# Kernel optimization log

Measured on AMD Instinct MI355X. Metric: run time of the kernel, lower is better.

The kernel has to match this reference:

```python
import jax, jax.numpy as jnp
import numpy as np

DIM = 512
NSLOTS = 8
ITERS = 3
EPS = 1e-8
LN_EPS = 1e-5
SCALE = DIM ** -0.5


def _ln(x, g, b):
    m = jnp.mean(x, axis=-1, keepdims=True)
    v = jnp.mean((x - m) ** 2, axis=-1, keepdims=True)
    return (x - m) / jnp.sqrt(v + LN_EPS) * g + b


def _gru(x, h, W_ih, W_hh, b_ih, b_hh):
    # PyTorch GRUCell, gate order r,z,n
    gi = x @ W_ih.T + b_ih
    gh = h @ W_hh.T + b_hh
    ir, iz, inn = jnp.split(gi, 3, axis=-1)
    hr, hz, hn = jnp.split(gh, 3, axis=-1)
    r = jax.nn.sigmoid(ir + hr)
    z = jax.nn.sigmoid(iz + hz)
    n = jnp.tanh(inn + r * hn)
    return (1.0 - z) * n + z * h


def _norm_attn(dots):
    # softmax over slot axis, then renormalize over token axis
    a = jax.nn.softmax(dots, axis=1)
    return a / (jnp.sum(a, axis=-1, keepdims=True) + EPS)


def setup_inputs() -> dict:
    key = jax.random.key(0)
    ks = jax.random.split(key, 16)
    b, na, ni = 32, 1024, 3136
    d, hd = DIM, DIM  # hidden_dim = max(dim, 128) = 512
    s = 0.02
    inp = {
        'inputs_audio': jax.random.normal(ks[0], (b, na, d), jnp.float32),
        'inputs_image': jax.random.normal(ks[1], (b, ni, d), jnp.float32),
        'slots_noise': jax.random.normal(ks[2], (b, NSLOTS, d), jnp.float32),
        'slots_mu': jax.random.normal(ks[3], (1, 1, d), jnp.float32),
        'slots_logsigma': jnp.zeros((1, 1, d), jnp.float32),
        'ln_in_g': jnp.ones((d,), jnp.float32), 'ln_in_b': jnp.zeros((d,), jnp.float32),
        'ln_slots_g': jnp.ones((d,), jnp.float32), 'ln_slots_b': jnp.zeros((d,), jnp.float32),
        'ln_ff_g': jnp.ones((d,), jnp.float32), 'ln_ff_b': jnp.zeros((d,), jnp.float32),
        'Wq': jax.random.normal(ks[4], (d, d), jnp.float32) * s, 'bq': jnp.zeros((d,), jnp.float32),
        'Wk': jax.random.normal(ks[5], (d, d), jnp.float32) * s, 'bk': jnp.zeros((d,), jnp.float32),
        'Wv': jax.random.normal(ks[6], (d, d), jnp.float32) * s, 'bv': jnp.zeros((d,), jnp.float32),
        'W_ih': jax.random.normal(ks[7], (3 * d, d), jnp.float32) * s,
        'W_hh': jax.random.normal(ks[8], (3 * d, d), jnp.float32) * s,
        'b_ih': jnp.zeros((3 * d,), jnp.float32), 'b_hh': jnp.zeros((3 * d,), jnp.float32),
        'W1': jax.random.normal(ks[9], (hd, d), jnp.float32) * s, 'b1': jnp.zeros((hd,), jnp.float32),
        'W2': jax.random.normal(ks[10], (d, hd), jnp.float32) * s, 'b2': jnp.zeros((d,), jnp.float32),
    }
    return inp


def reference(inputs_audio, inputs_image, slots_noise, slots_mu, slots_logsigma,
              ln_in_g, ln_in_b, ln_slots_g, ln_slots_b, ln_ff_g, ln_ff_b,
              Wq, bq, Wk, bk, Wv, bv, W_ih, W_hh, b_ih, b_hh, W1, b1, W2, b2):
    b, na, d = inputs_audio.shape
    slots0 = slots_mu + jnp.exp(slots_logsigma) * slots_noise  # [b, S, d]

    ia = _ln(inputs_audio, ln_in_g, ln_in_b)
    ii = _ln(inputs_image, ln_in_g, ln_in_b)
    k_a = ia @ Wk.T + bk
    v_a = ia @ Wv.T + bv
    k_i = ii @ Wk.T + bk
    v_i = ii @ Wv.T + bv

    def mlp(x):
        return jax.nn.relu(x @ W1.T + b1) @ W2.T + b2

    def step(slots, k, v):
        prev = slots
        sn = _ln(slots, ln_slots_g, ln_slots_b)
        q = sn @ Wq.T + bq
        dots = jnp.einsum('bid,bjd->bij', q, k) * SCALE
        attn = _norm_attn(dots)
        upd = jnp.einsum('bjd,bij->bid', v, attn)
        h = _gru(upd.reshape(-1, d), prev.reshape(-1, d), W_ih, W_hh, b_ih, b_hh)
        slots = h.reshape(b, -1, d)
        slots = slots + mlp(_ln(slots, ln_ff_g, ln_ff_b))
        return slots, q, attn

    slots_a, slots_i = slots0, slots0
    for _ in range(ITERS):
        slots_a, q_a, attn_a = step(slots_a, k_a, v_a)
        slots_i, q_i, attn_i = step(slots_i, k_i, v_i)

    cross_ai = _norm_attn(jnp.einsum('bid,bjd->bij', q_a, k_i) * SCALE)  # audio->image
    cross_ia = _norm_attn(jnp.einsum('bid,bjd->bij', q_i, k_a) * SCALE)  # image->audio

    return (slots_a, q_a, k_a, attn_a, cross_ia,
            slots_i, q_i, k_i, attn_i, cross_ai)
```

## Files before the change

kernel.cpp:

```cpp
#include <hip/hip_runtime.h>
#include <hip/hip_bf16.h>

#define DIM 512
#define EPS 1e-8f
#define LN_EPS 1e-5f
#define SCALE 0.04419417382415922f

typedef float f32x4 __attribute__((ext_vector_type(4)));
typedef __bf16 bf16;
typedef __bf16 bf16x8 __attribute__((ext_vector_type(8)));

typedef const __attribute__((address_space(1))) void gvoid;
typedef __attribute__((address_space(3))) void lvoid;

__device__ inline float bf2f_lo(unsigned u) { union { unsigned x; float f; } c; c.x = u << 16; return c.f; }
__device__ inline float bf2f_hi(unsigned u) { union { unsigned x; float f; } c; c.x = u & 0xffff0000u; return c.f; }

#define SBAR() do { __builtin_amdgcn_sched_barrier(0); \
                    __builtin_amdgcn_s_barrier(); \
                    __builtin_amdgcn_sched_barrier(0); } while (0)

__global__ __launch_bounds__(256) void k_stats_convert(
    const float* __restrict__ xa, const float* __restrict__ xi,
    bf16* __restrict__ xbfa, bf16* __restrict__ xbfi,
    float* __restrict__ sa, float* __restrict__ si, int MA)
{
  int row = blockIdx.x * 4 + (threadIdx.x >> 6);
  int lane = threadIdx.x & 63;
  bool isA = row < MA;
  int lrow = isA ? row : row - MA;
  const float* xr = (isA ? xa : xi) + (size_t)lrow * DIM;
  bf16* xbf = (isA ? xbfa : xbfi) + (size_t)lrow * DIM;
  float* stats = (isA ? sa : si) + (size_t)lrow * 2;
  float4 a = *(const float4*)(xr + lane * 8);
  float4 b = *(const float4*)(xr + lane * 8 + 4);
  float s  = a.x + a.y + a.z + a.w + b.x + b.y + b.z + b.w;
  float ss = a.x*a.x + a.y*a.y + a.z*a.z + a.w*a.w
           + b.x*b.x + b.y*b.y + b.z*b.z + b.w*b.w;
  for (int off = 32; off; off >>= 1) { s += __shfl_xor(s, off); ss += __shfl_xor(ss, off); }
  float mean = s * (1.0f / DIM);
  float var  = ss * (1.0f / DIM) - mean * mean;
  float rs   = rsqrtf(var + LN_EPS);
  if (lane == 0) { stats[0] = mean; stats[1] = rs; }
  union { bf16 h[8]; uint4 u; } cv;
  cv.h[0] = (bf16)a.x; cv.h[1] = (bf16)a.y; cv.h[2] = (bf16)a.z; cv.h[3] = (bf16)a.w;
  cv.h[4] = (bf16)b.x; cv.h[5] = (bf16)b.y; cv.h[6] = (bf16)b.z; cv.h[7] = (bf16)b.w;
  *(uint4*)(xbf + lane * 8) = cv.u;
}

__global__ __launch_bounds__(256) void k_stats512(
    const float* __restrict__ x, float* __restrict__ stats)
{
  int row = blockIdx.x * 4 + (threadIdx.x >> 6);
  int lane = threadIdx.x & 63;
  const float* xr = x + (size_t)row * DIM;
  float4 a = *(const float4*)(xr + lane * 8);
  float4 b = *(const float4*)(xr + lane * 8 + 4);
  float s  = a.x + a.y + a.z + a.w + b.x + b.y + b.z + b.w;
  float ss = a.x*a.x + a.y*a.y + a.z*a.z + a.w*a.w
           + b.x*b.x + b.y*b.y + b.z*b.z + b.w*b.w;
  for (int off = 32; off; off >>= 1) { s += __shfl_xor(s, off); ss += __shfl_xor(ss, off); }
  float mean = s * (1.0f / DIM);
  float rs   = rsqrtf(ss * (1.0f / DIM) - mean * mean + LN_EPS);
  if (lane == 0) { stats[row * 2] = mean; stats[row * 2 + 1] = rs; }
}

__global__ __launch_bounds__(64) void k_prep(
    const float* __restrict__ Wk, const float* __restrict__ bk,
    const float* __restrict__ Wv, const float* __restrict__ bv,
    const float* __restrict__ g_in, const float* __restrict__ b_in,
    const float* __restrict__ Wq, const float* __restrict__ bq,
    const float* __restrict__ g_s, const float* __restrict__ b_s,
    const float* __restrict__ W1, const float* __restrict__ b1,
    const float* __restrict__ g_f, const float* __restrict__ b_f,
    bf16* __restrict__ wbf, float* __restrict__ c1kv, float* __restrict__ c2kv,
    float* __restrict__ Wqp, float* __restrict__ cq1, float* __restrict__ cq2,
    float* __restrict__ W1p, float* __restrict__ cf1, float* __restrict__ cf2)
{
  int n = blockIdx.x; int lane = threadIdx.x;
  if (n < 1024) {
    const float* W = (n < DIM) ? (Wk + (size_t)n * DIM) : (Wv + (size_t)(n - DIM) * DIM);
    float bias = (n < DIM) ? bk[n] : bv[n - DIM];
    float s1 = 0.f, s2 = 0.f;
    union { bf16 h[8]; uint4 u; } cv;
#pragma unroll
    for (int j = 0; j < 8; ++j) {
      int d = lane * 8 + j;
      float w = W[d];
      float gw = g_in[d] * w;
      s1 += gw; s2 += b_in[d] * w;
      cv.h[j] = (bf16)gw;
    }
    *(uint4*)(wbf + (size_t)n * DIM + lane * 8) = cv.u;
    for (int off = 32; off; off >>= 1) { s1 += __shfl_xor(s1, off); s2 += __shfl_xor(s2, off); }
    if (lane == 0) { c1kv[n] = s1; c2kv[n] = s2 + bias; }
  } else {
    int m; const float* W; float bias; const float* g; const float* b;
    float* Wp; float* cc1; float* cc2;
    if (n < 1536) { m = n - 1024; W = Wq + (size_t)m * DIM; bias = bq[m]; g = g_s; b = b_s; Wp = Wqp; cc1 = cq1; cc2 = cq2; }
    else          { m = n - 1536; W = W1 + (size_t)m * DIM; bias = b1[m]; g = g_f; b = b_f; Wp = W1p; cc1 = cf1; cc2 = cf2; }
    float s1 = 0.f, s2 = 0.f;
    float arr[8];
#pragma unroll
    for (int j = 0; j < 8; ++j) {
      int d = lane * 8 + j;
      float w = W[d];
      float gw = g[d] * w;
      s1 += gw; s2 += b[d] * w;
      arr[j] = gw;
    }
    *(float4*)(Wp + (size_t)m * DIM + lane * 8)     = make_float4(arr[0], arr[1], arr[2], arr[3]);
    *(float4*)(Wp + (size_t)m * DIM + lane * 8 + 4) = make_float4(arr[4], arr[5], arr[6], arr[7]);
    for (int off = 32; off; off >>= 1) { s1 += __shfl_xor(s1, off); s2 += __shfl_xor(s2, off); }
    if (lane == 0) { cc1[m] = s1; cc2[m] = s2 + bias; }
  }
}

// ... 97 lines not shown
      pk.h[0] = (bf16)o.x; pk.h[1] = (bf16)o.y; pk.h[2] = (bf16)o.z; pk.h[3] = (bf16)o.w;
      if (col0 < DIM) {
        *(float4*)&kout[(size_t)row * DIM + col] = o;
        if (kbf) *(uint2*)&kbf[(size_t)row * DIM + col] = pk.u;
      } else {
        *(uint2*)&vbf[(size_t)row * DIM + (col - DIM)] = pk.u;
      }
    }
  }
}

__global__ __launch_bounds__(256) void k_f2bf(
    const float* __restrict__ in, bf16* __restrict__ out)
{
  size_t i = ((size_t)blockIdx.x * 256 + threadIdx.x) * 8;
  float4 a = *(const float4*)(in + i);
  float4 b = *(const float4*)(in + i + 4);
  union { bf16 h[8]; uint4 u; } cv;
  cv.h[0] = (bf16)a.x; cv.h[1] = (bf16)a.y; cv.h[2] = (bf16)a.z; cv.h[3] = (bf16)a.w;
  cv.h[4] = (bf16)b.x; cv.h[5] = (bf16)b.y; cv.h[6] = (bf16)b.z; cv.h[7] = (bf16)b.w;
  *(uint4*)(out + i) = cv.u;
}

__global__ __launch_bounds__(256) void k_init_slots(
    const float* __restrict__ noise, const float* __restrict__ mu,
    const float* __restrict__ lsig, float* __restrict__ slots,
    float* __restrict__ stats)
{
  int row = blockIdx.x;
  int t = threadIdx.x;
  int d1 = t + 256;
  float v0 = mu[t]  + expf(lsig[t])  * noise[row * DIM + t];
  float v1 = mu[d1] + expf(lsig[d1]) * noise[row * DIM + d1];
  slots[(size_t)row * DIM + t]  = v0;
  slots[(size_t)row * DIM + d1] = v1;
  slots[131072 + (size_t)row * DIM + t]  = v0;
  slots[131072 + (size_t)row * DIM + d1] = v1;
  float s = v0 + v1, ss = v0 * v0 + v1 * v1;
  for (int off = 32; off; off >>= 1) { s += __shfl_xor(s, off); ss += __shfl_xor(ss, off); }
  __shared__ float red[8];
  int wv = t >> 6, ln = t & 63;
  if (ln == 0) { red[wv] = s; red[4 + wv] = ss; }
  __syncthreads();
  if (t == 0) {
    s = red[0] + red[1] + red[2] + red[3];
    ss = red[4] + red[5] + red[6] + red[7];
    float mean = s * (1.0f / DIM);
    float rs = rsqrtf(ss * (1.0f / DIM) - mean * mean + LN_EPS);
    stats[row * 2] = mean; stats[row * 2 + 1] = rs;
    stats[(row + 256) * 2] = mean; stats[(row + 256) * 2 + 1] = rs;
  }
}

template <int MODE>
__global__ __launch_bounds__(128) void k_sgemm(
    const float* __restrict__ A, const float* __restrict__ B, int N,
    float* __restrict__ C,
    const float* __restrict__ c1a, const float* __restrict__ c2a,
    const float* __restrict__ stats,
    const float* __restrict__ bias, const float* __restrict__ invden,
    const float* __restrict__ R,
    float* __restrict__ outA, float* __restrict__ outI,
    bf16* __restrict__ qbf)
{
  __shared__ float As[32][33];
  __shared__ float Bs[64][33];
  int t = threadIdx.x;
  int m0 = blockIdx.y * 32, n0 = blockIdx.x * 64;
  float acc[4][4] = {};
  for (int k0 = 0; k0 < DIM; k0 += 32) {
    __syncthreads();
#pragma unroll
    for (int p = 0; p < 2; ++p) {
      int idx = p * 128 + t, r = idx >> 3, c4 = (idx & 7) * 4;
      float4 v = *(const float4*)(A + (size_t)(m0 + r) * DIM + k0 + c4);
      As[r][c4] = v.x; As[r][c4 + 1] = v.y; As[r][c4 + 2] = v.z; As[r][c4 + 3] = v.w;
    }
#pragma unroll
    for (int p = 0; p < 4; ++p) {
      int idx = p * 128 + t, r = idx >> 3, c4 = (idx & 7) * 4;
      float4 v = *(const float4*)(B + (size_t)(n0 + r) * DIM + k0 + c4);
      Bs[r][c4] = v.x; Bs[r][c4 + 1] = v.y; Bs[r][c4 + 2] = v.z; Bs[r][c4 + 3] = v.w;
    }
    __syncthreads();
    int tr = t >> 4, tc = t & 15;
#pragma unroll
    for (int k = 0; k < 32; ++k) {
      float a0 = As[tr * 4][k], a1 = As[tr * 4 + 1][k], a2 = As[tr * 4 + 2][k], a3 = As[tr * 4 + 3][k];
      float b0 = Bs[tc * 4][k], b1 = Bs[tc * 4 + 1][k], b2 = Bs[tc * 4 + 2][k], b3 = Bs[tc * 4 + 3][k];
      acc[0][0] += a0 * b0; acc[0][1] += a0 * b1; acc[0][2] += a0 * b2; acc[0][3] += a0 * b3;
      acc[1][0] += a1 * b0; acc[1][1] += a1 * b1; acc[1][2] += a1 * b2; acc[1][3] += a1 * b3;
      acc[2][0] += a2 * b0; acc[2][1] += a2 * b1; acc[2][2] += a2 * b2; acc[2][3] += a2 * b3;
      acc[3][0] += a3 * b0; acc[3][1] += a3 * b1; acc[3][2] += a3 * b2; acc[3][3] += a3 * b3;
    }
  }
  int tr = t >> 4, tc = t & 15;
#pragma unroll
  for (int mi = 0; mi < 4; ++mi) {
    int row = m0 + tr * 4 + mi;
#pragma unroll
    for (int ni = 0; ni < 4; ++ni) {
      int col = n0 + tc * 4 + ni;
      float v = acc[mi][ni];
      if (MODE == 0 || MODE == 3) {
        float mean = stats[row * 2], rs = stats[row * 2 + 1];
        v = rs * v - rs * mean * c1a[col] + c2a[col];
      }
      if (MODE == 4) v += bias[col];
      if (MODE == 3) v = fmaxf(v, 0.0f);
      if (MODE == 4) v += R[(size_t)row * N + col];
      if (MODE == 0) {
        if (outA) {
          if (row < 256) outA[(size_t)row * DIM + col] = v;
          else           outI[(size_t)(row - 256) * DIM + col] = v;
        }
        qbf[(size_t)row * DIM + col] = (bf16)(v * SCALE);
      } else {
        C[(size_t)row * N + col] = v;
        if (MODE == 4 && outA) {
          if (row < 256) outA[(size_t)row * DIM + col] = v;
          else           outI[(size_t)(row - 256) * DIM + col] = v;
        }
      }
    }
  }
}

__global__ __launch_bounds__(128) void k_gates(
    const float* __restrict__ num, const float* __restrict__ slots,
    const float* __restrict__ Wih, const float* __restrict__ Whh,
    const float* __restrict__ bih, const float* __restrict__ bhh,
    const float* __restrict__ invden,
    float* __restrict__ gib, float* __restrict__ ghb)
{
  bool first = blockIdx.x < 24;
  const float* A = first ? num : slots;
  const float* B = first ? Wih : Whh;
  const float* bias = first ? bih : bhh;
  float* C = first ? gib : ghb;
  int n0 = (first ? blockIdx.x : blockIdx.x - 24) * 64;
  int m0 = blockIdx.y * 32;
  __shared__ float As[32][33];
  __shared__ float Bs[64][33];
  int t = threadIdx.x;
  float acc[4][4] = {};
  for (int k0 = 0; k0 < DIM; k0 += 32) {
    __syncthreads();
#pragma unroll
    for (int p = 0; p < 2; ++p) {
      int idx = p * 128 + t, r = idx >> 3, c4 = (idx & 7) * 4;
      float4 v = *(const float4*)(A + (size_t)(m0 + r) * DIM + k0 + c4);
      As[r][c4] = v.x; As[r][c4 + 1] = v.y; As[r][c4 + 2] = v.z; As[r][c4 + 3] = v.w;
    }
#pragma unroll
    for (int p = 0; p < 4; ++p) {
      int idx = p * 128 + t, r = idx >> 3, c4 = (idx & 7) * 4;
      float4 v = *(const float4*)(B + (size_t)(n0 + r) * DIM + k0 + c4);
      Bs[r][c4] = v.x; Bs[r][c4 + 1] = v.y; Bs[r][c4 + 2] = v.z; Bs[r][c4 + 3] = v.w;
    }
    __syncthreads();
    int tr = t >> 4, tc = t & 15;
#pragma unroll
    for (int k = 0; k < 32; ++k) {
      float a0 = As[tr * 4][k], a1 = As[tr * 4 + 1][k], a2 = As[tr * 4 + 2][k], a3 = As[tr * 4 + 3][k];
      float b0 = Bs[tc * 4][k], b1 = Bs[tc * 4 + 1][k], b2 = Bs[tc * 4 + 2][k], b3 = Bs[tc * 4 + 3][k];
      acc[0][0] += a0 * b0; acc[0][1] += a0 * b1; acc[0][2] += a0 * b2; acc[0][3] += a0 * b3;
      acc[1][0] += a1 * b0; acc[1][1] += a1 * b1; acc[1][2] += a1 * b2; acc[1][3] += a1 * b3;
      acc[2][0] += a2 * b0; acc[2][1] += a2 * b1; acc[2][2] += a2 * b2; acc[2][3] += a2 * b3;
      acc[3][0] += a3 * b0; acc[3][1] += a3 * b1; acc[3][2] += a3 * b2; acc[3][3] += a3 * b3;
    }
  }
  int tr = t >> 4, tc = t & 15;
#pragma unroll
  for (int mi = 0; mi < 4; ++mi) {
    int row = m0 + tr * 4 + mi;
    float sc = first ? invden[row] : 1.0f;
#pragma unroll
    for (int ni = 0; ni < 4; ++ni) {
      int col = n0 + tc * 4 + ni;
      C[(size_t)row * 1536 + col] = acc[mi][ni] * sc + bias[col];
    }
  }
}

template <int LAST>
__global__ __launch_bounds__(256) void k_dots_upd(
    const bf16* __restrict__ qA, const bf16* __restrict__ qI,
    const bf16* __restrict__ kA, const bf16* __restrict__ kI,
    const bf16* __restrict__ vA, const bf16* __restrict__ vI,
    float* __restrict__ aoutA, float* __restrict__ aoutI,
    float* __restrict__ acA, float* __restrict__ acI,
    float* __restrict__ denp, float* __restrict__ denpc,
    float* __restrict__ numpA, float* __restrict__ numpI,
    int NA_, int NI_)
{
  __shared__ bf16 ks[2][128 * 64];
  __shared__ float ash[128 * 12];
  __shared__ float dsh[64];
  int t = threadIdx.x, wave = t >> 6, lane = t & 63;
  int b = blockIdx.y, tile = blockIdx.x;
  bool isA = tile < 8;
  int til = isA ? tile : tile - 8;
  int N = isA ? NA_ : NI_;
  int nc = isA ? 8 : 25;
  int j0 = til * 128;
  const bf16* qo = (isA ? qA : qI) + (size_t)b * 8 * DIM;
  const bf16* qc = (isA ? qI : qA) + (size_t)b * 8 * DIM;
  const bf16* k  = (isA ? kA : kI) + (size_t)b * N * DIM;
  const bf16* v  = (isA ? vA : vI) + (size_t)b * N * DIM;
  float* aout = (isA ? aoutA : aoutI) + (LAST ? (size_t)b * 8 * N : 0);
  float* aco  = (isA ? acA  : acI ) + (LAST ? (size_t)b * 8 * N : 0);
  int drow = (isA ? 0 : 256) + b * 8;

  const int l15 = lane & 15, q16 = lane >> 4;
  bf16x8 afq[16], afqc[16];
  {
    const bf16* qr = qo + (size_t)(l15 & 7) * DIM + q16 * 8;
#pragma unroll
    for (int f = 0; f < 16; ++f) afq[f] = *(const bf16x8*)(qr + f * 32);
  }
  if (LAST) {
    const bf16* qr = qc + (size_t)(l15 & 7) * DIM + q16 * 8;
#pragma unroll
    for (int f = 0; f < 16; ++f) afqc[f] = *(const bf16x8*)(qr + f * 32);
  }

  const int sr  = wave * 8 + (lane >> 3);
  const int sgl = ((lane & 7) ^ (lane >> 3)) * 8;
  int jr = j0 + sr; if (jr > N - 1) jr = N - 1;
  const bf16* ksrc = k + (size_t)jr * DIM + sgl;
  int jr2 = j0 + 32 + sr; if (jr2 > N - 1) jr2 = N - 1;
  const bf16* ksrc2 = k + (size_t)jr2 * DIM + sgl;
  int jr3 = j0 + 64 + sr; if (jr3 > N - 1) jr3 = N - 1;
// ... 83 lines not shown
    if (LAST) {
      float dv[8];
#pragma unroll
      for (int r = 0; r < 4; ++r) {
        float own = accc[n][r];
        float oth = __shfl_xor(own, 16);
        if (q16 == 0) { dv[r] = own; dv[4 + r] = oth; }
        else          { dv[r] = oth; dv[4 + r] = own; }
      }
      float mx = dv[0];
#pragma unroll
      for (int i = 1; i < 8; ++i) mx = fmaxf(mx, dv[i]);
      float sum = 0.f;
#pragma unroll
      for (int i = 0; i < 8; ++i) { dv[i] = __expf(dv[i] - mx); sum += dv[i]; }
      float inv = 1.0f / sum;
#pragma unroll
      for (int i = 0; i < 8; ++i) {
        float av = valid ? dv[i] * inv : 0.0f;
        dsumc[i] += av;
        if (q16 == 0 && valid) aco[(size_t)i * N + j] = av;
      }
    }
  }
#pragma unroll
  for (int i = 0; i < 8; ++i) {
    float x1 = dsum[i];
    x1 += __shfl_xor(x1, 1); x1 += __shfl_xor(x1, 2);
    x1 += __shfl_xor(x1, 4); x1 += __shfl_xor(x1, 8);
    dsum[i] = x1;
    if (LAST) {
      float x2 = dsumc[i];
      x2 += __shfl_xor(x2, 1); x2 += __shfl_xor(x2, 2);
      x2 += __shfl_xor(x2, 4); x2 += __shfl_xor(x2, 8);
      dsumc[i] = x2;
    }
  }
  if (lane == 0) {
#pragma unroll
    for (int i = 0; i < 8; ++i) {
      dsh[wave * 8 + i] = dsum[i];
      if (LAST) dsh[32 + wave * 8 + i] = dsumc[i];
    }
  }
  __syncthreads();
  if (t < 8) {
    denp[((size_t)drow + t) * 32 + til] = dsh[t] + dsh[8 + t] + dsh[16 + t] + dsh[24 + t];
  }
  if (LAST && t >= 8 && t < 16) {
    int i = t - 8;
    denpc[((size_t)drow + i) * 32 + til] = dsh[32 + i] + dsh[40 + i] + dsh[48 + i] + dsh[56 + i];
  }

  float ua[16] = {};
  int d0 = t * 2;
  for (int jj = 0; jj < 128; ++jj) {
    int jv = j0 + jj; if (jv > N - 1) jv = N - 1;
    unsigned vv = *(const unsigned*)(v + (size_t)jv * DIM + d0);
    float v0 = bf2f_lo(vv), v1 = bf2f_hi(vv);
    float4 a0 = *(const float4*)&ash[jj * 12];
    float4 a1 = *(const float4*)&ash[jj * 12 + 4];
    ua[0]  += a0.x * v0; ua[1]  += a0.x * v1;
    ua[2]  += a0.y * v0; ua[3]  += a0.y * v1;
    ua[4]  += a0.z * v0; ua[5]  += a0.z * v1;
    ua[6]  += a0.w * v0; ua[7]  += a0.w * v1;
    ua[8]  += a1.x * v0; ua[9]  += a1.x * v1;
    ua[10] += a1.y * v0; ua[11] += a1.y * v1;
    ua[12] += a1.z * v0; ua[13] += a1.z * v1;
    ua[14] += a1.w * v0; ua[15] += a1.w * v1;
  }
  float* np = (isA ? numpA : numpI) + (((size_t)b * nc + til) * 8) * DIM;
#pragma unroll
  for (int i = 0; i < 8; ++i)
    *(float2*)&np[(size_t)i * DIM + d0] = make_float2(ua[i * 2], ua[i * 2 + 1]);
}

__global__ __launch_bounds__(256) void k_numred(
    const float* __restrict__ numpA, const float* __restrict__ numpI,
    const float* __restrict__ denp,
    float* __restrict__ num, float* __restrict__ invden)
{
  int m = blockIdx.x, t = threadIdx.x;
  bool isA = m < 256;
  int mm = isA ? m : m - 256;
  int bb = mm >> 3, i = mm & 7;
  int nc = isA ? 8 : 25;
  const float* np = (isA ? numpA : numpI) + (((size_t)bb * nc) * 8 + i) * DIM;
  int d0 = t * 2;
  float s0 = 0.f, s1 = 0.f;
  for (int c = 0; c < nc; ++c) {
    float2 vv = *(const float2*)&np[(size_t)c * 8 * DIM + d0];
    s0 += vv.x; s1 += vv.y;
  }
  *(float2*)&num[(size_t)m * DIM + d0] = make_float2(s0, s1);
  if (t == 0) {
    float den = EPS;
    for (int c2 = 0; c2 < nc; ++c2) den += denp[(size_t)m * 32 + c2];
    invden[m] = 1.0f / den;
  }
}

__global__ __launch_bounds__(256) void k_gru(
    const float* __restrict__ gi, const float* __restrict__ gh,
    const float* __restrict__ prev,
    float* __restrict__ hout, float* __restrict__ stats_h)
{
  int m = blockIdx.x; int t = threadIdx.x;
  size_t b3 = (size_t)m * 1536, b1 = (size_t)m * DIM;
  float h[2]; float s = 0.f, ss = 0.f;
#pragma unroll
  for (int p = 0; p < 2; ++p) {
    int d = t + p * 256;
    float ir = gi[b3 + d], iz = gi[b3 + 512 + d], in_ = gi[b3 + 1024 + d];
    float hr = gh[b3 + d], hz = gh[b3 + 512 + d], hn = gh[b3 + 1024 + d];
    float r = 1.f / (1.f + __expf(-(ir + hr)));
    float z = 1.f / (1.f + __expf(-(iz + hz)));
    float n = tanhf(in_ + r * hn);
    float hv = (1.f - z) * n + z * prev[b1 + d];
    hout[b1 + d] = hv;
    h[p] = hv; s += hv; ss += hv * hv;
  }
  for (int off = 32; off; off >>= 1) { s += __shfl_xor(s, off); ss += __shfl_xor(ss, off); }
  __shared__ float red[8];
  int wv = t >> 6, ln = t & 63;
  if (ln == 0) { red[wv] = s; red[4 + wv] = ss; }
  __syncthreads();
  s = red[0] + red[1] + red[2] + red[3];
  ss = red[4] + red[5] + red[6] + red[7];
  float mean = s * (1.0f / DIM);
  float rs = rsqrtf(ss * (1.0f / DIM) - mean * mean + LN_EPS);
  if (t == 0) { stats_h[m * 2] = mean; stats_h[m * 2 + 1] = rs; }
}

__global__ __launch_bounds__(256) void k_renorm2(
    const float* __restrict__ aA, const float* __restrict__ aI,
    const float* __restrict__ denp,
    float* __restrict__ outA, float* __restrict__ outI, int NA_, int NI_)
{
  int m = blockIdx.x; int t = threadIdx.x;
  bool isA = m < 256;
  int mm = isA ? m : m - 256;
  int N = isA ? NA_ : NI_;
  int nch = isA ? 8 : 25;
  const float* in = (isA ? aA : aI) + (size_t)mm * N;
  float* out = (isA ? outA : outI) + (size_t)mm * N;
  float den = EPS;
  for (int c = 0; c < nch; ++c) den += denp[(size_t)m * 32 + c];
  float inv = 1.0f / den;
  for (int idx = t; idx * 4 < N; idx += 256) {
    float4 v = *(const float4*)&in[idx * 4];
    v.x *= inv; v.y *= inv; v.z *= inv; v.w *= inv;
    *(float4*)&out[idx * 4] = v;
  }
}

extern "C" void kernel_launch(void* const* d_in, const int* in_sizes, int n_in,
                              void* d_out, int out_size, void* d_ws, size_t ws_size,
                              hipStream_t stream)
{
  (void)in_sizes; (void)n_in; (void)out_size;
  const float* x_a   = (const float*)d_in[0];
  const float* x_i   = (const float*)d_in[1];
  const float* noise = (const float*)d_in[2];
  const float* mu    = (const float*)d_in[3];
  const float* lsig  = (const float*)d_in[4];
  const float* ln_in_g = (const float*)d_in[5];
  const float* ln_in_b = (const float*)d_in[6];
  const float* ln_s_g  = (const float*)d_in[7];
  const float* ln_s_b  = (const float*)d_in[8];
  const float* ln_f_g  = (const float*)d_in[9];
  const float* ln_f_b  = (const float*)d_in[10];
  const float* Wq = (const float*)d_in[11]; const float* bq = (const float*)d_in[12];
  const float* Wk = (const float*)d_in[13]; const float* bk = (const float*)d_in[14];
  const float* Wv = (const float*)d_in[15]; const float* bv = (const float*)d_in[16];
  const float* W_ih = (const float*)d_in[17]; const float* W_hh = (const float*)d_in[18];
  const float* b_ih = (const float*)d_in[19]; const float* b_hh = (const float*)d_in[20];
  const float* W1 = (const float*)d_in[21]; const float* b1 = (const float*)d_in[22];
  const float* W2 = (const float*)d_in[23]; const float* b2 = (const float*)d_in[24];

  const int NA = 1024, NI = 3136;
  const int MA = 32 * NA, MI = 32 * NI;

  float* out = (float*)d_out;
  float* o_slots_a  = out;
  float* o_q_a      = out + 131072;
  float* o_k_a      = out + 262144;
  float* o_attn_a   = out + 17039360;
  float* o_cross_ia = out + 17301504;
  float* o_slots_i  = out + 17563648;
  float* o_q_i      = out + 17694720;
  float* o_k_i      = out + 17825792;
  float* o_attn_i   = out + 69206016;
  float* o_cross_ai = out + 70008832;

  char* w = (char*)d_ws;
  size_t used = 0;
  auto alloc = [&](size_t bytes) {
    char* p = w + used;
    used += (bytes + 255) & ~(size_t)255;
    return p;
  };
  bf16* xbf_a = (bf16*)alloc((size_t)MA * DIM * 2);
  bf16* xbf_i = (bf16*)alloc((size_t)MI * DIM * 2);
  bf16* vbf_a = (bf16*)alloc((size_t)MA * DIM * 2);
  bf16* vbf_i = (bf16*)alloc((size_t)MI * DIM * 2);
  float* stats_a = (float*)alloc((size_t)MA * 2 * 4);
  float* stats_i = (float*)alloc((size_t)MI * 2 * 4);
  bf16* wbf  = (bf16*)alloc(1024 * 512 * 2);
  float* c1kv = (float*)alloc(1024 * 4);
  float* c2kv = (float*)alloc(1024 * 4);
  float* Wqp = (float*)alloc(512 * 512 * 4);
  float* cq1 = (float*)alloc(512 * 4);
  float* cq2 = (float*)alloc(512 * 4);
  float* W1p = (float*)alloc(512 * 512 * 4);
  float* cf1 = (float*)alloc(512 * 4);
  float* cf2 = (float*)alloc(512 * 4);
  float* slots = (float*)alloc(512 * 512 * 4);
  bf16*  qbf   = (bf16*)alloc(512 * 512 * 2);
  float* mid   = (float*)alloc(512 * 512 * 4);
  float* hid   = (float*)alloc(512 * 512 * 4);
  float* num   = (float*)alloc(512 * 512 * 4);
  float* gib   = (float*)alloc(512 * 1536 * 4);
  float* ghb   = (float*)alloc(512 * 1536 * 4);
  float* stats_s = (float*)alloc(512 * 2 * 4);
  float* stats_h = (float*)alloc(512 * 2 * 4);
  float* invden  = (float*)alloc(512 * 4);
  float* denp    = (float*)alloc(512 * 32 * 4);
  float* denpc   = (float*)alloc(512 * 32 * 4);
  float* abuf_a  = (float*)alloc((size_t)256 * NA * 4);
  float* abuf_i  = (float*)alloc((size_t)256 * NI * 4);
  float* abufc_a = (float*)alloc((size_t)256 * NA * 4);
  float* abufc_i = (float*)alloc((size_t)256 * NI * 4);
  float* numpA   = (float*)alloc((size_t)32 * 8 * 8 * DIM * 4);
  float* numpI   = (float*)alloc((size_t)32 * 25 * 8 * DIM * 4);
  if (used > ws_size) return;

  size_t kbf_bytes = (((size_t)MA * DIM * 2 + 255) & ~(size_t)255)
                   + (((size_t)MI * DIM * 2 + 255) & ~(size_t)255);
  bf16* kbf_a; bf16* kbf_i; bool kbf_fused;
  if (used + kbf_bytes <= ws_size) {
    kbf_a = (bf16*)alloc((size_t)MA * DIM * 2);
    kbf_i = (bf16*)alloc((size_t)MI * DIM * 2);
    kbf_fused = true;
  } else {
    kbf_a = xbf_a; kbf_i = xbf_i;
    kbf_fused = false;
  }

  k_stats_convert<<<(MA + MI) / 4, 256, 0, stream>>>(x_a, x_i, xbf_a, xbf_i,
                                                     stats_a, stats_i, MA);
  k_prep<<<2048, 64, 0, stream>>>(Wk, bk, Wv, bv, ln_in_g, ln_in_b,
                                  Wq, bq, ln_s_g, ln_s_b, W1, b1, ln_f_g, ln_f_b,
                                  wbf, c1kv, c2kv, Wqp, cq1, cq2, W1p, cf1, cf2);
  {
    int nblkA = (MA / 128) * 8;
    int nblkTot = nblkA + (MI / 128) * 8;
    k_kv_gemm<<<nblkTot, 256, 0, stream>>>(xbf_a, xbf_i, wbf, stats_a, stats_i,
        c1kv, c2kv, o_k_a, o_k_i,
        kbf_fused ? kbf_a : nullptr, kbf_fused ? kbf_i : nullptr,
        vbf_a, vbf_i, nblkA, nblkTot);
  }
  if (!kbf_fused) {
    k_f2bf<<<MA * DIM / 2048, 256, 0, stream>>>(o_k_a, kbf_a);
    k_f2bf<<<MI * DIM / 2048, 256, 0, stream>>>(o_k_i, kbf_i);
  }
  k_init_slots<<<256, 256, 0, stream>>>(noise, mu, lsig, slots, stats_s);

  for (int it = 0; it < 3; ++it) {
    bool last = (it == 2);
    k_sgemm<0><<<dim3(8, 16), 128, 0, stream>>>(slots, Wqp, DIM, nullptr,
        cq1, cq2, stats_s, nullptr, nullptr, nullptr,
        last ? o_q_a : nullptr, last ? o_q_i : nullptr, qbf);
    if (!last)
      k_dots_upd<0><<<dim3(33, 32), 256, 0, stream>>>(qbf, qbf + 256 * DIM,
          kbf_a, kbf_i, vbf_a, vbf_i,
          nullptr, nullptr, nullptr, nullptr, denp, nullptr,
          numpA, numpI, NA, NI);
    else
      k_dots_upd<1><<<dim3(33, 32), 256, 0, stream>>>(qbf, qbf + 256 * DIM,
          kbf_a, kbf_i, vbf_a, vbf_i,
          abuf_a, abuf_i, abufc_a, abufc_i, denp, denpc,
          numpA, numpI, NA, NI);
    k_numred<<<512, 256, 0, stream>>>(numpA, numpI, denp, num, invden);
    k_gates<<<dim3(48, 16), 128, 0, stream>>>(num, slots, W_ih, W_hh,
        b_ih, b_hh, invden, gib, ghb);
    k_gru<<<512, 256, 0, stream>>>(gib, ghb, slots, mid, stats_h);
    k_sgemm<3><<<dim3(8, 16), 128, 0, stream>>>(mid, W1p, DIM, hid,
        cf1, cf2, stats_h, nullptr, nullptr, nullptr, nullptr, nullptr, nullptr);
    k_sgemm<4><<<dim3(8, 16), 128, 0, stream>>>(hid, W2, DIM, slots,
        nullptr, nullptr, nullptr, b2, nullptr, mid,
        last ? o_slots_a : nullptr, last ? o_slots_i : nullptr, nullptr);
    if (!last) k_stats512<<<128, 256, 0, stream>>>(slots, stats_s);
  }

  k_renorm2<<<512, 256, 0, stream>>>(abuf_a, abuf_i, denp, o_attn_a, o_attn_i, NA, NI);
  k_renorm2<<<512, 256, 0, stream>>>(abufc_a, abufc_i, denpc, o_cross_ia, o_cross_ai, NA, NI);
}
```

Baseline: 1.104 ms.

## Fuse per-iteration slot update chain into one persistent kernel with grid barriers

Replaces the numred, gates, GRU, two MLP GEMMs, stats and next-iteration Q GEMM launches with a single 256-block persistent kernel that separates phases with atomic-counter grid barriers. The Q projection for the next iteration is folded into the end of the chain, and the first Q GEMM is hoisted before the loop. The goal is to remove several small kernel launches and their gaps per iteration. The cost is spin-wait barriers that assume all 256 blocks are co-resident, plus smaller 32x64 tiles with 2 outputs per thread, which leave many blocks idle in the 128-tile phases.

```diff
diff --git a/kernel.cpp b/kernel.cpp
--- a/kernel.cpp
+++ b/kernel.cpp
@@ -19,6 +19,17 @@
 #define SBAR() do { __builtin_amdgcn_sched_barrier(0); \
                     __builtin_amdgcn_s_barrier(); \
                     __builtin_amdgcn_sched_barrier(0); } while (0)
+
+__device__ inline void gsync(unsigned* bar) {
+  __syncthreads();
+  __threadfence();
+  if (threadIdx.x == 0) {
+    atomicAdd(bar, 1u);
+    while (atomicAdd(bar, 0u) < 256u) __builtin_amdgcn_s_sleep(2);
+  }
+  __syncthreads();
+  __threadfence();
+}
 
 __global__ __launch_bounds__(256) void k_stats_convert(
     const float* __restrict__ xa, const float* __restrict__ xi,
@@ -46,23 +57,6 @@
   cv.h[0] = (bf16)a.x; cv.h[1] = (bf16)a.y; cv.h[2] = (bf16)a.z; cv.h[3] = (bf16)a.w;
   cv.h[4] = (bf16)b.x; cv.h[5] = (bf16)b.y; cv.h[6] = (bf16)b.z; cv.h[7] = (bf16)b.w;
   *(uint4*)(xbf + lane * 8) = cv.u;
-}
-
-__global__ __launch_bounds__(256) void k_stats512(
-    const float* __restrict__ x, float* __restrict__ stats)
-{
-  int row = blockIdx.x * 4 + (threadIdx.x >> 6);
-  int lane = threadIdx.x & 63;
-  const float* xr = x + (size_t)row * DIM;
-  float4 a = *(const float4*)(xr + lane * 8);
-  float4 b = *(const float4*)(xr + lane * 8 + 4);
-  float s  = a.x + a.y + a.z + a.w + b.x + b.y + b.z + b.w;
-  float ss = a.x*a.x + a.y*a.y + a.z*a.z + a.w*a.w
-           + b.x*b.x + b.y*b.y + b.z*b.z + b.w*b.w;
-  for (int off = 32; off; off >>= 1) { s += __shfl_xor(s, off); ss += __shfl_xor(ss, off); }
-  float mean = s * (1.0f / DIM);
-  float rs   = rsqrtf(ss * (1.0f / DIM) - mean * mean + LN_EPS);
-  if (lane == 0) { stats[row * 2] = mean; stats[row * 2 + 1] = rs; }
 }
 
 __global__ __launch_bounds__(64) void k_prep(
@@ -266,16 +260,10 @@
   }
 }
 
-template <int MODE>
-__global__ __launch_bounds__(128) void k_sgemm(
-    const float* __restrict__ A, const float* __restrict__ B, int N,
-    float* __restrict__ C,
+__global__ __launch_bounds__(128) void k_qgemm(
+    const float* __restrict__ A, const float* __restrict__ B,
     const float* __restrict__ c1a, const float* __restrict__ c2a,
-    const float* __restrict__ stats,
-    const float* __restrict__ bias, const float* __restrict__ invden,
-    const float* __restrict__ R,
-    float* __restrict__ outA, float* __restrict__ outI,
-    bf16* __restrict__ qbf)
+    const float* __restrict__ stats, bf16* __restrict__ qbf)
 {
   __shared__ float As[32][33];
   __shared__ float Bs[64][33];
@@ -312,87 +300,232 @@
 #pragma unroll
   for (int mi = 0; mi < 4; ++mi) {
     int row = m0 + tr * 4 + mi;
+    float mean = stats[row * 2], rs = stats[row * 2 + 1];
 #pragma unroll
     for (int ni = 0; ni < 4; ++ni) {
       int col = n0 + tc * 4 + ni;
-      float v = acc[mi][ni];
-      if (MODE == 0 || MODE == 3) {
-        float mean = stats[row * 2], rs = stats[row * 2 + 1];
-        v = rs * v - rs * mean * c1a[col] + c2a[col];
+      float v = rs * acc[mi][ni] - rs * mean * c1a[col] + c2a[col];
+      qbf[(size_t)row * DIM + col] = (bf16)(v * SCALE);
+    }
+  }
+}
+
+__device__ inline void mm32x64(
+    const float* __restrict__ A, const float* __restrict__ B,
+    int m0, int n0, float acc[4][2],
+    float (*As)[33], float (*Bs)[33])
+{
+  int t = threadIdx.x;
+#pragma unroll
+  for (int i = 0; i < 4; ++i) { acc[i][0] = 0.f; acc[i][1] = 0.f; }
+  for (int k0 = 0; k0 < DIM; k0 += 32) {
+    __syncthreads();
+    {
+      int r = t >> 3, c4 = (t & 7) * 4;
+      float4 v = *(const float4*)(A + (size_t)(m0 + r) * DIM + k0 + c4);
+      As[r][c4] = v.x; As[r][c4 + 1] = v.y; As[r][c4 + 2] = v.z; As[r][c4 + 3] = v.w;
+    }
+#pragma unroll
+    for (int p = 0; p < 2; ++p) {
+      int idx = p * 256 + t, r = idx >> 3, c4 = (idx & 7) * 4;
+      float4 v = *(const float4*)(B + (size_t)(n0 + r) * DIM + k0 + c4);
+      Bs[r][c4] = v.x; Bs[r][c4 + 1] = v.y; Bs[r][c4 + 2] = v.z; Bs[r][c4 + 3] = v.w;
+    }
+    __syncthreads();
+    int tr = t >> 5, tc = t & 31;
+#pragma unroll
+    for (int k = 0; k < 32; ++k) {
+      float a0 = As[tr * 4][k], a1 = As[tr * 4 + 1][k];
+      float a2 = As[tr * 4 + 2][k], a3 = As[tr * 4 + 3][k];
+      float b0 = Bs[tc * 2][k], b1 = Bs[tc * 2 + 1][k];
+      acc[0][0] += a0 * b0; acc[0][1] += a0 * b1;
+      acc[1][0] += a1 * b0; acc[1][1] += a1 * b1;
+      acc[2][0] += a2 * b0; acc[2][1] += a2 * b1;
+      acc[3][0] += a3 * b0; acc[3][1] += a3 * b1;
+    }
+  }
+}
+
+template <int CMODE>
+__global__ __launch_bounds__(256) void k_chain(
+    const float* __restrict__ numpA, const float* __restrict__ numpI,
+    const float* __restrict__ denp,
+    float* __restrict__ num, float* __restrict__ invden,
+    const float* __restrict__ Wih, const float* __restrict__ Whh,
+    const float* __restrict__ bih, const float* __restrict__ bhh,
+    float* __restrict__ gib, float* __restrict__ ghb,
+    float* __restrict__ slots, float* __restrict__ mid,
+    float* __restrict__ stats_h,
+    const float* __restrict__ W1p, const float* __restrict__ cf1,
+    const float* __restrict__ cf2, float* __restrict__ hid,
+    const float* __restrict__ W2, const float* __restrict__ b2,
+    const float* __restrict__ Wqp, const float* __restrict__ cq1,
+    const float* __restrict__ cq2,
+    float* __restrict__ stats_s, bf16* __restrict__ qbf,
+    float* __restrict__ o_slots_a, float* __restrict__ o_slots_i,
+    float* __restrict__ o_q_a, float* __restrict__ o_q_i,
+    unsigned* __restrict__ bar)
+{
+  __shared__ float As[32][33];
+  __shared__ float Bs[64][33];
+  __shared__ float red[8];
+  int t = threadIdx.x;
+
+  {
+    int r0 = blockIdx.x * 2;
+    for (int r = r0; r < r0 + 2; ++r) {
+      bool isA = r < 256;
+      int mm = isA ? r : r - 256;
+      int bb = mm >> 3, i = mm & 7;
+      int nc = isA ? 8 : 25;
+      const float* np = (isA ? numpA : numpI) + (((size_t)bb * nc) * 8 + i) * DIM;
+      int d0 = t * 2;
+      float s0 = 0.f, s1 = 0.f;
+      for (int c = 0; c < nc; ++c) {
+        float2 vv = *(const float2*)&np[(size_t)c * 8 * DIM + d0];
+        s0 += vv.x; s1 += vv.y;
       }
-      if (MODE == 4) v += bias[col];
-      if (MODE == 3) v = fmaxf(v, 0.0f);
-      if (MODE == 4) v += R[(size_t)row * N + col];
-      if (MODE == 0) {
-        if (outA) {
-          if (row < 256) outA[(size_t)row * DIM + col] = v;
-          else           outI[(size_t)(row - 256) * DIM + col] = v;
-        }
+      *(float2*)&num[(size_t)r * DIM + d0] = make_float2(s0, s1);
+      if (t == 0) {
+        float den = EPS;
+        for (int c2 = 0; c2 < nc; ++c2) den += denp[(size_t)r * 32 + c2];
+        invden[r] = 1.0f / den;
+      }
+    }
+  }
+  gsync(bar + 0);
+
+  for (int vt = blockIdx.x; vt < 768; vt += 256) {
+    bool first = vt < 384;
+    int lv = first ? vt : vt - 384;
+    int m0 = (lv / 24) * 32, n0 = (lv % 24) * 64;
+    const float* Aa = first ? num : slots;
+    const float* Bb = first ? Wih : Whh;
+    const float* bias = first ? bih : bhh;
+    float* C = first ? gib : ghb;
+    float acc[4][2];
+    mm32x64(Aa, Bb, m0, n0, acc, As, Bs);
+    int tr = t >> 5, tc = t & 31;
+#pragma unroll
+    for (int i = 0; i < 4; ++i) {
+      int row = m0 + tr * 4 + i;
+      float sc = first ? invden[row] : 1.0f;
+      float2 o = make_float2(acc[i][0] * sc + bias[n0 + tc * 2],
+                             acc[i][1] * sc + bias[n0 + tc * 2 + 1]);
+      *(float2*)&C[(size_t)row * 1536 + n0 + tc * 2] = o;
+    }
+  }
+  gsync(bar + 1);
+
+  for (int rr = 0; rr < 2; ++rr) {
+    int m = blockIdx.x * 2 + rr;
+    size_t b3 = (size_t)m * 1536, b1 = (size_t)m * DIM;
+    float h[2]; float s = 0.f, ss = 0.f;
+#pragma unroll
+    for (int p = 0; p < 2; ++p) {
+      int d = t + p * 256;
+      float ir = gib[b3 + d], iz = gib[b3 + 512 + d], in_ = gib[b3 + 1024 + d];
+      float hr = ghb[b3 + d], hz = ghb[b3 + 512 + d], hn = ghb[b3 + 1024 + d];
+      float r = 1.f / (1.f + __expf(-(ir + hr)));
+      float z = 1.f / (1.f + __expf(-(iz + hz)));
+      float n = tanhf(in_ + r * hn);
+      float hv = (1.f - z) * n + z * slots[b1 + d];
+      mid[b1 + d] = hv;
+      h[p] = hv; s += hv; ss += hv * hv;
+    }
+    for (int off = 32; off; off >>= 1) { s += __shfl_xor(s, off); ss += __shfl_xor(ss, off); }
+    int wv = t >> 6, ln = t & 63;
+    if (ln == 0) { red[wv] = s; red[4 + wv] = ss; }
+    __syncthreads();
+    if (t == 0) {
+      s = red[0] + red[1] + red[2] + red[3];
+      ss = red[4] + red[5] + red[6] + red[7];
+      float mean = s * (1.0f / DIM);
+      float rs = rsqrtf(ss * (1.0f / DIM) - mean * mean + LN_EPS);
+      stats_h[m * 2] = mean; stats_h[m * 2 + 1] = rs;
+    }
+    __syncthreads();
+  }
+  gsync(bar + 2);
+
+  for (int vt = blockIdx.x; vt < 128; vt += 256) {
+    int m0 = (vt >> 3) * 32, n0 = (vt & 7) * 64;
+    float acc[4][2];
+    mm32x64(mid, W1p, m0, n0, acc, As, Bs);
+    int tr = t >> 5, tc = t & 31;
+#pragma unroll
+    for (int i = 0; i < 4; ++i) {
+      int row = m0 + tr * 4 + i;
+      float mean = stats_h[row * 2], rs = stats_h[row * 2 + 1];
+      float2 o;
+      o.x = fmaxf(rs * acc[i][0] - rs * mean * cf1[n0 + tc * 2]     + cf2[n0 + tc * 2],     0.f);
+      o.y = fmaxf(rs * acc[i][1] - rs * mean * cf1[n0 + tc * 2 + 1] + cf2[n0 + tc * 2 + 1], 0.f);
+      *(float2*)&hid[(size_t)row * DIM + n0 + tc * 2] = o;
+    }
+  }
+  gsync(bar + 3);
+
+  for (int vt = blockIdx.x; vt < 128; vt += 256) {
+    int m0 = (vt >> 3) * 32, n0 = (vt & 7) * 64;
+    float acc[4][2];
+    mm32x64(hid, W2, m0, n0, acc, As, Bs);
+    int tr = t >> 5, tc = t & 31;
+#pragma unroll
+    for (int i = 0; i < 4; ++i) {
+      int row = m0 + tr * 4 + i;
+      int col = n0 + tc * 2;
+      float2 rmid = *(const float2*)&mid[(size_t)row * DIM + col];
+      float2 o = make_float2(acc[i][0] + b2[col] + rmid.x,
+                             acc[i][1] + b2[col + 1] + rmid.y);
+      *(float2*)&slots[(size_t)row * DIM + col] = o;
+      if (CMODE == 2) {
+        if (row < 256) *(float2*)&o_slots_a[(size_t)row * DIM + col] = o;
+        else           *(float2*)&o_slots_i[(size_t)(row - 256) * DIM + col] = o;
+      }
+    }
+  }
+  if (CMODE == 2) return;
+  gsync(bar + 4);
+
+  for (int rr = 0; rr < 2; ++rr) {
+    int m = blockIdx.x * 2 + rr;
+    const float* xr = slots + (size_t)m * DIM;
+    float v0 = xr[t], v1 = xr[t + 256];
+    float s = v0 + v1, ss = v0 * v0 + v1 * v1;
+    for (int off = 32; off; off >>= 1) { s += __shfl_xor(s, off); ss += __shfl_xor(ss, off); }
+    int wv = t >> 6, ln = t & 63;
+    if (ln == 0) { red[wv] = s; red[4 + wv] = ss; }
+    __syncthreads();
+    if (t == 0) {
+      s = red[0] + red[1] + red[2] + red[3];
+      ss = red[4] + red[5] + red[6] + red[7];
+      float mean = s * (1.0f / DIM);
+      float rs = rsqrtf(ss * (1.0f / DIM) - mean * mean + LN_EPS);
+      stats_s[m * 2] = mean; stats_s[m * 2 + 1] = rs;
+    }
+    __syncthreads();
+  }
+  gsync(bar + 5);
+
+  for (int vt = blockIdx.x; vt < 128; vt += 256) {
+    int m0 = (vt >> 3) * 32, n0 = (vt & 7) * 64;
+    float acc[4][2];
+    mm32x64(slots, Wqp, m0, n0, acc, As, Bs);
+    int tr = t >> 5, tc = t & 31;
+#pragma unroll
+    for (int i = 0; i < 4; ++i) {
+      int row = m0 + tr * 4 + i;
+      float mean = stats_s[row * 2], rs = stats_s[row * 2 + 1];
+#pragma unroll
+      for (int j = 0; j < 2; ++j) {
+        int col = n0 + tc * 2 + j;
+        float v = rs * acc[i][j] - rs * mean * cq1[col] + cq2[col];
         qbf[(size_t)row * DIM + col] = (bf16)(v * SCALE);
-      } else {
-        C[(size_t)row * N + col] = v;
-        if (MODE == 4 && outA) {
-          if (row < 256) outA[(size_t)row * DIM + col] = v;
-          else           outI[(size_t)(row - 256) * DIM + col] = v;
+        if (CMODE == 1) {
+          if (row < 256) o_q_a[(size_t)row * DIM + col] = v;
+          else           o_q_i[(size_t)(row - 256) * DIM + col] = v;
         }
       }
-    }
-  }
-}
-
-__global__ __launch_bounds__(128) void k_gates(
-    const float* __restrict__ num, const float* __restrict__ slots,
-    const float* __restrict__ Wih, const float* __restrict__ Whh,
-    const float* __restrict__ bih, const float* __restrict__ bhh,
-    const float* __restrict__ invden,
-    float* __restrict__ gib, float* __restrict__ ghb)
-{
-  bool first = blockIdx.x < 24;
-  const float* A = first ? num : slots;
-  const float* B = first ? Wih : Whh;
-  const float* bias = first ? bih : bhh;
-  float* C = first ? gib : ghb;
-  int n0 = (first ? blockIdx.x : blockIdx.x - 24) * 64;
-  int m0 = blockIdx.y * 32;
-  __shared__ float As[32][33];
-  __shared__ float Bs[64][33];
-  int t = threadIdx.x;
-  float acc[4][4] = {};
-  for (int k0 = 0; k0 < DIM; k0 += 32) {
-    __syncthreads();
-#pragma unroll
-    for (int p = 0; p < 2; ++p) {
-      int idx = p * 128 + t, r = idx >> 3, c4 = (idx & 7) * 4;
-      float4 v = *(const float4*)(A + (size_t)(m0 + r) * DIM + k0 + c4);
-      As[r][c4] = v.x; As[r][c4 + 1] = v.y; As[r][c4 + 2] = v.z; As[r][c4 + 3] = v.w;
-    }
-#pragma unroll
-    for (int p = 0; p < 4; ++p) {
-      int idx = p * 128 + t, r = idx >> 3, c4 = (idx & 7) * 4;
-      float4 v = *(const float4*)(B + (size_t)(n0 + r) * DIM + k0 + c4);
-      Bs[r][c4] = v.x; Bs[r][c4 + 1] = v.y; Bs[r][c4 + 2] = v.z; Bs[r][c4 + 3] = v.w;
-    }
-    __syncthreads();
-    int tr = t >> 4, tc = t & 15;
-#pragma unroll
-    for (int k = 0; k < 32; ++k) {
-      float a0 = As[tr * 4][k], a1 = As[tr * 4 + 1][k], a2 = As[tr * 4 + 2][k], a3 = As[tr * 4 + 3][k];
-      float b0 = Bs[tc * 4][k], b1 = Bs[tc * 4 + 1][k], b2 = Bs[tc * 4 + 2][k], b3 = Bs[tc * 4 + 3][k];
-      acc[0][0] += a0 * b0; acc[0][1] += a0 * b1; acc[0][2] += a0 * b2; acc[0][3] += a0 * b3;
-      acc[1][0] += a1 * b0; acc[1][1] += a1 * b1; acc[1][2] += a1 * b2; acc[1][3] += a1 * b3;
-      acc[2][0] += a2 * b0; acc[2][1] += a2 * b1; acc[2][2] += a2 * b2; acc[2][3] += a2 * b3;
-      acc[3][0] += a3 * b0; acc[3][1] += a3 * b1; acc[3][2] += a3 * b2; acc[3][3] += a3 * b3;
-    }
-  }
-  int tr = t >> 4, tc = t & 15;
-#pragma unroll
-  for (int mi = 0; mi < 4; ++mi) {
-    int row = m0 + tr * 4 + mi;
-    float sc = first ? invden[row] : 1.0f;
-#pragma unroll
-    for (int ni = 0; ni < 4; ++ni) {
-      int col = n0 + tc * 4 + ni;
-      C[(size_t)row * 1536 + col] = acc[mi][ni] * sc + bias[col];
     }
   }
 }
@@ -603,63 +736,6 @@
 #pragma unroll
   for (int i = 0; i < 8; ++i)
     *(float2*)&np[(size_t)i * DIM + d0] = make_float2(ua[i * 2], ua[i * 2 + 1]);
-}
-
-__global__ __launch_bounds__(256) void k_numred(
-    const float* __restrict__ numpA, const float* __restrict__ numpI,
-    const float* __restrict__ denp,
-    float* __restrict__ num, float* __restrict__ invden)
-{
-  int m = blockIdx.x, t = threadIdx.x;
-  bool isA = m < 256;
-  int mm = isA ? m : m - 256;
-  int bb = mm >> 3, i = mm & 7;
-  int nc = isA ? 8 : 25;
-  const float* np = (isA ? numpA : numpI) + (((size_t)bb * nc) * 8 + i) * DIM;
-  int d0 = t * 2;
-  float s0 = 0.f, s1 = 0.f;
-  for (int c = 0; c < nc; ++c) {
-    float2 vv = *(const float2*)&np[(size_t)c * 8 * DIM + d0];
-    s0 += vv.x; s1 += vv.y;
-  }
-  *(float2*)&num[(size_t)m * DIM + d0] = make_float2(s0, s1);
-  if (t == 0) {
-    float den = EPS;
-    for (int c2 = 0; c2 < nc; ++c2) den += denp[(size_t)m * 32 + c2];
-    invden[m] = 1.0f / den;
-  }
-}
-
-__global__ __launch_bounds__(256) void k_gru(
-    const float* __restrict__ gi, const float* __restrict__ gh,
-    const float* __restrict__ prev,
-    float* __restrict__ hout, float* __restrict__ stats_h)
-{
-  int m = blockIdx.x; int t = threadIdx.x;
-  size_t b3 = (size_t)m * 1536, b1 = (size_t)m * DIM;
-  float h[2]; float s = 0.f, ss = 0.f;
-#pragma unroll
-  for (int p = 0; p < 2; ++p) {
-    int d = t + p * 256;
-    float ir = gi[b3 + d], iz = gi[b3 + 512 + d], in_ = gi[b3 + 1024 + d];
-    float hr = gh[b3 + d], hz = gh[b3 + 512 + d], hn = gh[b3 + 1024 + d];
-    float r = 1.f / (1.f + __expf(-(ir + hr)));
-    float z = 1.f / (1.f + __expf(-(iz + hz)));
-    float n = tanhf(in_ + r * hn);
-    float hv = (1.f - z) * n + z * prev[b1 + d];
-    hout[b1 + d] = hv;
-    h[p] = hv; s += hv; ss += hv * hv;
-  }
-  for (int off = 32; off; off >>= 1) { s += __shfl_xor(s, off); ss += __shfl_xor(ss, off); }
-  __shared__ float red[8];
-  int wv = t >> 6, ln = t & 63;
-  if (ln == 0) { red[wv] = s; red[4 + wv] = ss; }
-  __syncthreads();
-  s = red[0] + red[1] + red[2] + red[3];
-  ss = red[4] + red[5] + red[6] + red[7];
-  float mean = s * (1.0f / DIM);
-  float rs = rsqrtf(ss * (1.0f / DIM) - mean * mean + LN_EPS);
-  if (t == 0) { stats_h[m * 2] = mean; stats_h[m * 2 + 1] = rs; }
 }
 
 __global__ __launch_bounds__(256) void k_renorm2(
@@ -757,6 +833,7 @@
   float* invden  = (float*)alloc(512 * 4);
   float* denp    = (float*)alloc(512 * 32 * 4);
   float* denpc   = (float*)alloc(512 * 32 * 4);
+  unsigned* bar  = (unsigned*)alloc(3 * 8 * 4);
   float* abuf_a  = (float*)alloc((size_t)256 * NA * 4);
   float* abuf_i  = (float*)alloc((size_t)256 * NI * 4);
   float* abufc_a = (float*)alloc((size_t)256 * NA * 4);
@@ -795,12 +872,11 @@
     k_f2bf<<<MI * DIM / 2048, 256, 0, stream>>>(o_k_i, kbf_i);
   }
   k_init_slots<<<256, 256, 0, stream>>>(noise, mu, lsig, slots, stats_s);
+  hipMemsetAsync(bar, 0, 3 * 8 * 4, stream);
+  k_qgemm<<<dim3(8, 16), 128, 0, stream>>>(slots, Wqp, cq1, cq2, stats_s, qbf);
 
   for (int it = 0; it < 3; ++it) {
     bool last = (it == 2);
-    k_sgemm<0><<<dim3(8, 16), 128, 0, stream>>>(slots, Wqp, DIM, nullptr,
-        cq1, cq2, stats_s, nullptr, nullptr, nullptr,
-        last ? o_q_a : nullptr, last ? o_q_i : nullptr, qbf);
     if (!last)
       k_dots_upd<0><<<dim3(33, 32), 256, 0, stream>>>(qbf, qbf + 256 * DIM,
           kbf_a, kbf_i, vbf_a, vbf_i,
@@ -811,16 +887,21 @@
           kbf_a, kbf_i, vbf_a, vbf_i,
           abuf_a, abuf_i, abufc_a, abufc_i, denp, denpc,
           numpA, numpI, NA, NI);
-    k_numred<<<512, 256, 0, stream>>>(numpA, numpI, denp, num, invden);
-    k_gates<<<dim3(48, 16), 128, 0, stream>>>(num, slots, W_ih, W_hh,
-        b_ih, b_hh, invden, gib, ghb);
-    k_gru<<<512, 256, 0, stream>>>(gib, ghb, slots, mid, stats_h);
-    k_sgemm<3><<<dim3(8, 16), 128, 0, stream>>>(mid, W1p, DIM, hid,
-        cf1, cf2, stats_h, nullptr, nullptr, nullptr, nullptr, nullptr, nullptr);
-    k_sgemm<4><<<dim3(8, 16), 128, 0, stream>>>(hid, W2, DIM, slots,
-        nullptr, nullptr, nullptr, b2, nullptr, mid,
-        last ? o_slots_a : nullptr, last ? o_slots_i : nullptr, nullptr);
-    if (!last) k_stats512<<<128, 256, 0, stream>>>(slots, stats_s);
+    if (it == 0)
+      k_chain<0><<<256, 256, 0, stream>>>(numpA, numpI, denp, num, invden,
+          W_ih, W_hh, b_ih, b_hh, gib, ghb, slots, mid, stats_h,
+          W1p, cf1, cf2, hid, W2, b2, Wqp, cq1, cq2, stats_s, qbf,
+          nullptr, nullptr, nullptr, nullptr, bar + 0);
+    else if (it == 1)
+      k_chain<1><<<256, 256, 0, stream>>>(numpA, numpI, denp, num, invden,
+          W_ih, W_hh, b_ih, b_hh, gib, ghb, slots, mid, stats_h,
+          W1p, cf1, cf2, hid, W2, b2, Wqp, cq1, cq2, stats_s, qbf,
+          nullptr, nullptr, o_q_a, o_q_i, bar + 8);
+    else
+      k_chain<2><<<256, 256, 0, stream>>>(numpA, numpI, denp, num, invden,
+          W_ih, W_hh, b_ih, b_hh, gib, ghb, slots, mid, stats_h,
+          W1p, cf1, cf2, hid, W2, b2, Wqp, cq1, cq2, stats_s, qbf,
+          o_slots_a, o_slots_i, nullptr, nullptr, bar + 16);
   }
 
   k_renorm2<<<512, 256, 0, stream>>>(abuf_a, abuf_i, denp, o_attn_a, o_attn_i, NA, NI);
```

New measurement: 1.910 ms. 73.0% more time.

## Widen per-thread V loads in attn·V and merge the two renorm launches

Applied to the files above, without the earlier changes.

The attention-times-values accumulation now splits the 128 tokens across four row groups of threads. Each thread loads 8 bf16 values at once with a 16-byte load and keeps an 8x8 register accumulator. The four partial sums are then reduced through shared memory that reuses the ks buffer, and the result is written as float4 stores. The intent is to replace the narrow 4-byte strided loads with wide coalesced ones and add ILP, at the cost of more registers, two extra barrier rounds and an LDS reduction. Separately, the two final renormalisation launches are fused into one launch with a 2-D grid to save launch overhead.

```diff
diff --git a/kernel.cpp b/kernel.cpp
--- a/kernel.cpp
+++ b/kernel.cpp
@@ -582,27 +582,55 @@
     denpc[((size_t)drow + i) * 32 + til] = dsh[32 + i] + dsh[40 + i] + dsh[48 + i] + dsh[56 + i];
   }
 
-  float ua[16] = {};
-  int d0 = t * 2;
-  for (int jj = 0; jj < 128; ++jj) {
+  int dg = t & 63, rg = t >> 6;
+  float ua[8][8];
+#pragma unroll
+  for (int i = 0; i < 8; ++i)
+#pragma unroll
+    for (int j = 0; j < 8; ++j) ua[i][j] = 0.f;
+  for (int jj = rg; jj < 128; jj += 4) {
     int jv = j0 + jj; if (jv > N - 1) jv = N - 1;
-    unsigned vv = *(const unsigned*)(v + (size_t)jv * DIM + d0);
-    float v0 = bf2f_lo(vv), v1 = bf2f_hi(vv);
+    uint4 vv = *(const uint4*)(v + (size_t)jv * DIM + dg * 8);
+    float vf[8];
+    vf[0] = bf2f_lo(vv.x); vf[1] = bf2f_hi(vv.x);
+    vf[2] = bf2f_lo(vv.y); vf[3] = bf2f_hi(vv.y);
+    vf[4] = bf2f_lo(vv.z); vf[5] = bf2f_hi(vv.z);
+    vf[6] = bf2f_lo(vv.w); vf[7] = bf2f_hi(vv.w);
     float4 a0 = *(const float4*)&ash[jj * 12];
     float4 a1 = *(const float4*)&ash[jj * 12 + 4];
-    ua[0]  += a0.x * v0; ua[1]  += a0.x * v1;
-    ua[2]  += a0.y * v0; ua[3]  += a0.y * v1;
-    ua[4]  += a0.z * v0; ua[5]  += a0.z * v1;
-    ua[6]  += a0.w * v0; ua[7]  += a0.w * v1;
-    ua[8]  += a1.x * v0; ua[9]  += a1.x * v1;
-    ua[10] += a1.y * v0; ua[11] += a1.y * v1;
-    ua[12] += a1.z * v0; ua[13] += a1.z * v1;
-    ua[14] += a1.w * v0; ua[15] += a1.w * v1;
-  }
+    float aw[8] = {a0.x, a0.y, a0.z, a0.w, a1.x, a1.y, a1.z, a1.w};
+#pragma unroll
+    for (int i = 0; i < 8; ++i)
+#pragma unroll
+      for (int j = 0; j < 8; ++j)
+        ua[i][j] += aw[i] * vf[j];
+  }
+  float* red2 = (float*)&ks[0][0];
   float* np = (isA ? numpA : numpI) + (((size_t)b * nc + til) * 8) * DIM;
 #pragma unroll
-  for (int i = 0; i < 8; ++i)
-    *(float2*)&np[(size_t)i * DIM + d0] = make_float2(ua[i * 2], ua[i * 2 + 1]);
+  for (int sg = 0; sg < 2; ++sg) {
+    __syncthreads();
+#pragma unroll
+    for (int i4 = 0; i4 < 4; ++i4) {
+      int i = sg * 4 + i4;
+      *(float4*)&red2[(i4 * 4 + rg) * 512 + dg * 8]     = make_float4(ua[i][0], ua[i][1], ua[i][2], ua[i][3]);
+      *(float4*)&red2[(i4 * 4 + rg) * 512 + dg * 8 + 4] = make_float4(ua[i][4], ua[i][5], ua[i][6], ua[i][7]);
+    }
+    __syncthreads();
+    {
+      int i4r = t >> 6;
+      int d0r = (t & 63) * 8;
+      float o[8];
+#pragma unroll
+      for (int j = 0; j < 8; ++j) {
+        int d = d0r + j;
+        o[j] = red2[(i4r * 4 + 0) * 512 + d] + red2[(i4r * 4 + 1) * 512 + d]
+             + red2[(i4r * 4 + 2) * 512 + d] + red2[(i4r * 4 + 3) * 512 + d];
+      }
+      *(float4*)&np[(size_t)(sg * 4 + i4r) * DIM + d0r]     = make_float4(o[0], o[1], o[2], o[3]);
+      *(float4*)&np[(size_t)(sg * 4 + i4r) * DIM + d0r + 4] = make_float4(o[4], o[5], o[6], o[7]);
+    }
+  }
 }
 
 __global__ __launch_bounds__(256) void k_numred(
@@ -664,18 +692,22 @@
 
 __global__ __launch_bounds__(256) void k_renorm2(
     const float* __restrict__ aA, const float* __restrict__ aI,
-    const float* __restrict__ denp,
-    float* __restrict__ outA, float* __restrict__ outI, int NA_, int NI_)
+    const float* __restrict__ acA, const float* __restrict__ acI,
+    const float* __restrict__ denp, const float* __restrict__ denpc,
+    float* __restrict__ oaA, float* __restrict__ oaI,
+    float* __restrict__ ocIA, float* __restrict__ ocAI, int NA_, int NI_)
 {
   int m = blockIdx.x; int t = threadIdx.x;
+  bool cr = blockIdx.y != 0;
   bool isA = m < 256;
   int mm = isA ? m : m - 256;
   int N = isA ? NA_ : NI_;
   int nch = isA ? 8 : 25;
-  const float* in = (isA ? aA : aI) + (size_t)mm * N;
-  float* out = (isA ? outA : outI) + (size_t)mm * N;
+  const float* in = (cr ? (isA ? acA : acI) : (isA ? aA : aI)) + (size_t)mm * N;
+  const float* dp = cr ? denpc : denp;
+  float* out = (cr ? (isA ? ocIA : ocAI) : (isA ? oaA : oaI)) + (size_t)mm * N;
   float den = EPS;
-  for (int c = 0; c < nch; ++c) den += denp[(size_t)m * 32 + c];
+  for (int c = 0; c < nch; ++c) den += dp[(size_t)m * 32 + c];
   float inv = 1.0f / den;
   for (int idx = t; idx * 4 < N; idx += 256) {
     float4 v = *(const float4*)&in[idx * 4];
@@ -823,6 +855,6 @@
     if (!last) k_stats512<<<128, 256, 0, stream>>>(slots, stats_s);
   }
 
-  k_renorm2<<<512, 256, 0, stream>>>(abuf_a, abuf_i, denp, o_attn_a, o_attn_i, NA, NI);
-  k_renorm2<<<512, 256, 0, stream>>>(abufc_a, abufc_i, denpc, o_cross_ia, o_cross_ai, NA, NI);
-}
+  k_renorm2<<<dim3(512, 2), 256, 0, stream>>>(abuf_a, abuf_i, abufc_a, abufc_i,
+      denp, denpc, o_attn_a, o_attn_i, o_cross_ia, o_cross_ai, NA, NI);
+}
```

Result: no change. 1.103 ms (median of 2 runs) (-0.1%).
